# Performance work log

Measured on AMD Instinct MI355X. Metric: run time of the kernel, lower is better.

Reference implementation:

```python
import jax, jax.numpy as jnp
import numpy as np

DECAY = 0.9
EPS = 1e-5


def setup_inputs() -> dict:
    key = jax.random.key(0)
    k1, k2, k3 = jax.random.split(key, 3)
    N, D, K = 262144, 492, 40
    return {
        "inputs": jax.random.normal(k1, (N, D), dtype=jnp.float32),
        "embedding_weight": jax.random.normal(k2, (K, D), dtype=jnp.float32),
        "ema_w": jax.random.normal(k3, (K, D), dtype=jnp.float32),
        "ema_cluster_size": jnp.zeros((K,), dtype=jnp.float32),
    }


def reference(inputs, embedding_weight, ema_w, ema_cluster_size):
    K, D = embedding_weight.shape
    flat = inputs.reshape(-1, D)  # [N, D]
    # squared L2 distances to each codebook entry: [N, K]
    distances = (
        jnp.sum(flat * flat, axis=1, keepdims=True)
        + jnp.sum(embedding_weight * embedding_weight, axis=1)
        - 2.0 * flat @ embedding_weight.T
    )
    idx = jnp.argmin(distances, axis=1)  # [N] nearest-code indices
    # one-hot column sums == per-code counts; encodings.T @ flat == segment sum
    counts = jax.ops.segment_sum(jnp.ones_like(idx, dtype=flat.dtype), idx, num_segments=K)
    dw = jax.ops.segment_sum(flat, idx, num_segments=K)  # [K, D]
    # EMA cluster-size update + Laplace smoothing
    cs = ema_cluster_size * DECAY + (1.0 - DECAY) * counts
    n = jnp.sum(cs)
    cs = (cs + EPS) / (n + K * EPS) * n
    # EMA codebook weight update
    new_ema_w = ema_w * DECAY + (1.0 - DECAY) * dw
    new_embedding = new_ema_w / cs[:, None]
    # quantize with the UPDATED codebook (as the torch code does)
    quantized = new_embedding[idx].reshape(inputs.shape)
    loss_vq = jnp.mean((quantized - inputs) ** 2)
    return loss_vq
```

## Files before the change

### kernel.cpp

```cpp
#include <hip/hip_runtime.h>

#define D 492
#define KC 40
#define DECAY 0.9f
#define EPS 1e-5f
#define PSPREAD 64

typedef __attribute__((ext_vector_type(8))) short bf16x8;
typedef __attribute__((ext_vector_type(4))) float f32x4;

__device__ __forceinline__ unsigned short f2bf(float f) {
  unsigned u = __float_as_uint(f);
  return (unsigned short)((u + 0x7fffu + ((u >> 16) & 1u)) >> 16);
}

__global__ void vq_sqnorm(const float* __restrict__ emb, float* __restrict__ sq) {
  int k = blockIdx.x;
  int lane = threadIdx.x;
  float s = 0.f;
  for (int d = lane; d < D; d += 64) {
    float v = emb[k * D + d];
    s = fmaf(v, v, s);
  }
  #pragma unroll
  for (int off = 32; off; off >>= 1) s += __shfl_down(s, off, 64);
  if (lane == 0) sq[k] = s;
}

__global__ __launch_bounds__(256, 3) void vq_assign(
    const float* __restrict__ x, const float* __restrict__ emb,
    const float* __restrict__ sq, int* __restrict__ idxp,
    float* __restrict__ counts, float* __restrict__ sumsq) {
  __shared__ unsigned short As[256 * 40];
  __shared__ unsigned short Bs[48 * 40];
  __shared__ float sq_s[KC];
  __shared__ float lcnt[KC];
  __shared__ float lss[4];
  int t = threadIdx.x;
  long row0 = (long)blockIdx.x * 256;
  if (t < KC) { sq_s[t] = sq[t]; lcnt[t] = 0.f; }
  float ss = 0.f;
  f32x4 acc[4][3];
  #pragma unroll
  for (int m = 0; m < 4; m++)
    #pragma unroll
    for (int n = 0; n < 3; n++) acc[m][n] = (f32x4){0.f, 0.f, 0.f, 0.f};

  int w = t >> 6, L = t & 63;
  int lm = L & 15, kq = L >> 4;

  for (int step = 0; step < 16; step++) {
    int kbase = step * 32;
    #pragma unroll
    for (int i = 0; i < 8; i++) {
      int j = t + i * 256;
      int r = j >> 3, c4 = j & 7;
      int col = kbase + c4 * 4;
      float4 v = make_float4(0.f, 0.f, 0.f, 0.f);
      if (col < D) v = *(const float4*)&x[(row0 + r) * D + col];
      ss = fmaf(v.x, v.x, fmaf(v.y, v.y, fmaf(v.z, v.z, fmaf(v.w, v.w, ss))));
      ushort4 u = { f2bf(v.x), f2bf(v.y), f2bf(v.z), f2bf(v.w) };
      *(ushort4*)&As[r * 40 + c4 * 4] = u;
    }
    {
      int n = t >> 3, c4 = t & 7;
      int col = kbase + c4 * 4;
      float4 v = make_float4(0.f, 0.f, 0.f, 0.f);
      if (n < KC && col < D) v = *(const float4*)&emb[n * D + col];
      ushort4 u = { f2bf(v.x), f2bf(v.y), f2bf(v.z), f2bf(v.w) };
      *(ushort4*)&Bs[n * 40 + c4 * 4] = u;
      if (t < 128) {
        int j = t + 256;
        n = j >> 3; c4 = j & 7;
        col = kbase + c4 * 4;
        v = make_float4(0.f, 0.f, 0.f, 0.f);
        if (n < KC && col < D) v = *(const float4*)&emb[n * D + col];
        ushort4 u2 = { f2bf(v.x), f2bf(v.y), f2bf(v.z), f2bf(v.w) };
        *(ushort4*)&Bs[n * 40 + c4 * 4] = u2;
      }
    }
    __syncthreads();
    bf16x8 a[4], b[3];
    #pragma unroll
    for (int m = 0; m < 4; m++)
      a[m] = *(const bf16x8*)&As[(w * 64 + m * 16 + lm) * 40 + kq * 8];
    #pragma unroll
    for (int n = 0; n < 3; n++)
      b[n] = *(const bf16x8*)&Bs[(n * 16 + lm) * 40 + kq * 8];
    #pragma unroll
    for (int m = 0; m < 4; m++)
      #pragma unroll
      for (int n = 0; n < 3; n++)
        acc[m][n] = __builtin_amdgcn_mfma_f32_16x16x32_bf16(a[m], b[n], acc[m][n], 0, 0, 0);
    __syncthreads();
  }

  #pragma unroll
  for (int m = 0; m < 4; m++) {
    #pragma unroll
    for (int reg = 0; reg < 4; reg++) {
      float best = 3.4e38f; int bi = 0;
      #pragma unroll
      for (int n = 0; n < 3; n++) {
        int col = n * 16 + lm;
        if (col < KC) {
          float v = sq_s[col] - 2.f * acc[m][n][reg];
          if (v < best || (v == best && col < bi)) { best = v; bi = col; }
        }
      }
      #pragma unroll
      for (int off = 1; off < 16; off <<= 1) {
        float ov = __shfl_xor(best, off, 64);
        int oi = __shfl_xor(bi, off, 64);
        if (ov < best || (ov == best && oi < bi)) { best = ov; bi = oi; }
      }
      if (lm == 0) {
        int r = w * 64 + m * 16 + kq * 4 + reg;
        idxp[row0 + r] = bi;
        atomicAdd(&lcnt[bi], 1.f);
      }
    }
  }
  #pragma unroll
  for (int off = 32; off; off >>= 1) ss += __shfl_down(ss, off, 64);
  if (L == 0) lss[w] = ss;
  __syncthreads();
  if (t == 0) atomicAdd(sumsq, lss[0] + lss[1] + lss[2] + lss[3]);
  if (t < KC) atomicAdd(&counts[t], lcnt[t]);
}

__global__ __launch_bounds__(128) void vq_dw(
    const float* __restrict__ x, const int* __restrict__ idxp,
    float* __restrict__ dwp) {
  __shared__ int cnt[KC], base[KC], pos[KC];
  __shared__ unsigned short order[512];
  int t = threadIdx.x;
  long row0 = (long)blockIdx.x * 512;
  if (t < KC) cnt[t] = 0;
  __syncthreads();
  int myk[4];
  #pragma unroll
  for (int u = 0; u < 4; u++) {
    myk[u] = idxp[row0 + t + u * 128];
    atomicAdd(&cnt[myk[u]], 1);
  }
  __syncthreads();
  if (t == 0) {
    int s = 0;
    for (int k = 0; k < KC; k++) { base[k] = s; pos[k] = s; s += cnt[k]; }
  }
  __syncthreads();
  #pragma unroll
  for (int u = 0; u < 4; u++) {
    int p = atomicAdd(&pos[myk[u]], 1);
    order[p] = (unsigned short)((t + u * 128) | (myk[u] << 9));
  }
  __syncthreads();

  int c = 4 * t;
  bool act = c < D;
  float* dst = dwp + (long)(blockIdx.x & (PSPREAD - 1)) * (KC * D);
  float4 a = make_float4(0.f, 0.f, 0.f, 0.f);
  int kcur = -1;

  int pk[8], pk2[8];
  float4 v[8], v2[8];
  #pragma unroll
  for (int u = 0; u < 8; u++) pk[u] = order[u];
  #pragma unroll
  for (int u = 0; u < 8; u++)
    v[u] = act ? *(const float4*)&x[(row0 + (pk[u] & 511)) * D + c]
               : make_float4(0.f, 0.f, 0.f, 0.f);

  for (int j0 = 0; j0 < 512; j0 += 8) {
    if (j0 + 8 < 512) {
      #pragma unroll
      for (int u = 0; u < 8; u++) pk2[u] = order[j0 + 8 + u];
      #pragma unroll
      for (int u = 0; u < 8; u++)
        v2[u] = act ? *(const float4*)&x[(row0 + (pk2[u] & 511)) * D + c]
                    : make_float4(0.f, 0.f, 0.f, 0.f);
    }
    #pragma unroll
    for (int u = 0; u < 8; u++) {
      int k = pk[u] >> 9;
      if (k != kcur) {
        if (kcur >= 0 && act) {
          atomicAdd(&dst[kcur * D + c], a.x);
          atomicAdd(&dst[kcur * D + c + 1], a.y);
          atomicAdd(&dst[kcur * D + c + 2], a.z);
          atomicAdd(&dst[kcur * D + c + 3], a.w);
        }
        a = v[u]; kcur = k;
      } else {
        a.x += v[u].x; a.y += v[u].y; a.z += v[u].z; a.w += v[u].w;
      }
    }
    #pragma unroll
    for (int u = 0; u < 8; u++) { pk[u] = pk2[u]; v[u] = v2[u]; }
  }
  if (kcur >= 0 && act) {
    atomicAdd(&dst[kcur * D + c], a.x);
    atomicAdd(&dst[kcur * D + c + 1], a.y);
    atomicAdd(&dst[kcur * D + c + 2], a.z);
    atomicAdd(&dst[kcur * D + c + 3], a.w);
  }
}

__global__ __launch_bounds__(256) void vq_reduce(
    const float* __restrict__ dwp, float* __restrict__ dw) {
  int i = blockIdx.x * 256 + threadIdx.x;
  if (i >= KC * D) return;
  float s = 0.f;
  #pragma unroll 8
  for (int cpy = 0; cpy < PSPREAD; cpy++) s += dwp[cpy * (KC * D) + i];
  dw[i] = s;
}

__global__ __launch_bounds__(256) void vq_final(
    const float* __restrict__ ema_w, const float* __restrict__ ema_cs,
    const float* __restrict__ counts, const float* __restrict__ dw,
    const float* __restrict__ sumsq, float* __restrict__ out, long NDl) {
  __shared__ float lcs[KC], lcnt[KC];
  __shared__ float r1[4], r2[4];
  int t = threadIdx.x;
  if (t < KC) {
    float c = counts[t];
    lcnt[t] = c;
    lcs[t] = ema_cs[t] * DECAY + (1.f - DECAY) * c;
  }
  __syncthreads();
  if (t == 0) {
    float n = 0.f;
    for (int k = 0; k < KC; k++) n += lcs[k];
    for (int k = 0; k < KC; k++) lcs[k] = (lcs[k] + EPS) / (n + KC * EPS) * n;
  }
  __syncthreads();
  float t1 = 0.f, t2 = 0.f;
  for (int i = t; i < KC * D; i += 256) {
    float dwv = dw[i];
    int k = i / D;
    float E = (DECAY * ema_w[i] + (1.f - DECAY) * dwv) / lcs[k];
    t1 = fmaf(lcnt[k] * E, E, t1);
    t2 = fmaf(E, dwv, t2);
  }
  #pragma unroll
  for (int off = 32; off; off >>= 1) {
    t1 += __shfl_down(t1, off, 64);
    t2 += __shfl_down(t2, off, 64);
  }
  int lane = t & 63, w = t >> 6;
  if (lane == 0) { r1[w] = t1; r2[w] = t2; }
  __syncthreads();
  if (t == 0) {
    double T1 = (double)r1[0] + r1[1] + r1[2] + r1[3];
    double T2 = (double)r2[0] + r2[1] + r2[2] + r2[3];
    double L = ((double)sumsq[0] - 2.0 * T2 + T1) / (double)NDl;
    out[0] = (float)L;
  }
}

extern "C" void kernel_launch(void* const* d_in, const int* in_sizes, int n_in,
                              void* d_out, int out_size, void* d_ws, size_t ws_size,
                              hipStream_t stream) {
  const float* x = (const float*)d_in[0];
  const float* emb = (const float*)d_in[1];
  const float* ema_w = (const float*)d_in[2];
  const float* ema_cs = (const float*)d_in[3];
  float* out = (float*)d_out;
  long NDl = (long)in_sizes[0];
  int N = (int)(NDl / D);

  char* ws = (char*)d_ws;
  float* sq = (float*)ws;
  float* counts = (float*)(ws + 256);
  float* sumsq = (float*)(ws + 512);
  float* dw = (float*)(ws + 1024);
  size_t part_off = 1024 + (size_t)KC * D * 4;
  part_off = (part_off + 255) & ~(size_t)255;
  float* dwp = (float*)(ws + part_off);
  size_t idx_off = part_off + (size_t)PSPREAD * KC * D * 4;
  int* idxp = (int*)(ws + idx_off);

  hipMemsetAsync(ws + 256, 0, 768, stream);
  hipMemsetAsync(ws + part_off, 0, (size_t)PSPREAD * KC * D * 4, stream);

  vq_sqnorm<<<KC, 64, 0, stream>>>(emb, sq);
  vq_assign<<<N / 256, 256, 0, stream>>>(x, emb, sq, idxp, counts, sumsq);
  vq_dw<<<N / 512, 128, 0, stream>>>(x, idxp, dwp);
  vq_reduce<<<(KC * D + 255) / 256, 256, 0, stream>>>(dwp, dw);
  vq_final<<<1, 256, 0, stream>>>(ema_w, ema_cs, counts, dw, sumsq, out, NDl);
}
```

Baseline: 920.3 us.

## Load MFMA operands directly from global, pre-convert codebook to padded bf16

Adds a prep kernel that converts the codebook to a zero-padded bf16 layout (512 columns, 48 rows) alongside the squared norms. The assign kernel then drops its LDS staging and per-step barriers, with each lane loading its x fragment straight from global memory into registers and the B fragments from the pre-converted buffer. This removes shared-memory traffic, barriers and repeated fp32-to-bf16 conversion of the codebook. In exchange, x is read with strided, less coalesced per-lane accesses, and launch bounds are relaxed from 3 to 2 blocks per SM.

After: 1.128 ms. 1.23x slower.

```diff
diff --git a/kernel.cpp b/kernel.cpp
--- a/kernel.cpp
+++ b/kernel.cpp
@@ -14,31 +14,49 @@
   return (unsigned short)((u + 0x7fffu + ((u >> 16) & 1u)) >> 16);
 }
 
-__global__ void vq_sqnorm(const float* __restrict__ emb, float* __restrict__ sq) {
+__global__ void vq_prep(const float* __restrict__ emb, float* __restrict__ sq,
+                        unsigned short* __restrict__ embb) {
   int k = blockIdx.x;
   int lane = threadIdx.x;
+  int c0 = lane * 8;
   float s = 0.f;
-  for (int d = lane; d < D; d += 64) {
-    float v = emb[k * D + d];
-    s = fmaf(v, v, s);
-  }
+  float v[8];
+  #pragma unroll
+  for (int j = 0; j < 8; j++) {
+    int c = c0 + j;
+    float f = (k < KC && c < D) ? emb[k * D + c] : 0.f;
+    v[j] = f;
+    s = fmaf(f, f, s);
+  }
+  bf16x8 u;
+  #pragma unroll
+  for (int j = 0; j < 8; j++) u[j] = (short)f2bf(v[j]);
+  *(bf16x8*)&embb[k * 512 + c0] = u;
   #pragma unroll
   for (int off = 32; off; off >>= 1) s += __shfl_down(s, off, 64);
-  if (lane == 0) sq[k] = s;
-}
-
-__global__ __launch_bounds__(256, 3) void vq_assign(
-    const float* __restrict__ x, const float* __restrict__ emb,
+  if (k < KC && lane == 0) sq[k] = s;
+}
+
+__global__ __launch_bounds__(256, 2) void vq_assign(
+    const float* __restrict__ x, const unsigned short* __restrict__ embb,
     const float* __restrict__ sq, int* __restrict__ idxp,
     float* __restrict__ counts, float* __restrict__ sumsq) {
-  __shared__ unsigned short As[256 * 40];
-  __shared__ unsigned short Bs[48 * 40];
   __shared__ float sq_s[KC];
   __shared__ float lcnt[KC];
   __shared__ float lss[4];
   int t = threadIdx.x;
   long row0 = (long)blockIdx.x * 256;
   if (t < KC) { sq_s[t] = sq[t]; lcnt[t] = 0.f; }
+
+  int w = t >> 6, L = t & 63;
+  int lm = L & 15, kq = L >> 4;
+
+  const float* xr[4];
+  #pragma unroll
+  for (int m = 0; m < 4; m++)
+    xr[m] = x + (row0 + w * 64 + m * 16 + lm) * (long)D + kq * 8;
+  const unsigned short* bp = embb + lm * 512 + kq * 8;
+
   float ss = 0.f;
   f32x4 acc[4][3];
   #pragma unroll
@@ -46,54 +64,72 @@
     #pragma unroll
     for (int n = 0; n < 3; n++) acc[m][n] = (f32x4){0.f, 0.f, 0.f, 0.f};
 
-  int w = t >> 6, L = t & 63;
-  int lm = L & 15, kq = L >> 4;
-
-  for (int step = 0; step < 16; step++) {
-    int kbase = step * 32;
-    #pragma unroll
-    for (int i = 0; i < 8; i++) {
-      int j = t + i * 256;
-      int r = j >> 3, c4 = j & 7;
-      int col = kbase + c4 * 4;
-      float4 v = make_float4(0.f, 0.f, 0.f, 0.f);
-      if (col < D) v = *(const float4*)&x[(row0 + r) * D + col];
-      ss = fmaf(v.x, v.x, fmaf(v.y, v.y, fmaf(v.z, v.z, fmaf(v.w, v.w, ss))));
-      ushort4 u = { f2bf(v.x), f2bf(v.y), f2bf(v.z), f2bf(v.w) };
-      *(ushort4*)&As[r * 40 + c4 * 4] = u;
-    }
-    {
-      int n = t >> 3, c4 = t & 7;
-      int col = kbase + c4 * 4;
-      float4 v = make_float4(0.f, 0.f, 0.f, 0.f);
-      if (n < KC && col < D) v = *(const float4*)&emb[n * D + col];
-      ushort4 u = { f2bf(v.x), f2bf(v.y), f2bf(v.z), f2bf(v.w) };
-      *(ushort4*)&Bs[n * 40 + c4 * 4] = u;
-      if (t < 128) {
-        int j = t + 256;
-        n = j >> 3; c4 = j & 7;
-        col = kbase + c4 * 4;
-        v = make_float4(0.f, 0.f, 0.f, 0.f);
-        if (n < KC && col < D) v = *(const float4*)&emb[n * D + col];
-        ushort4 u2 = { f2bf(v.x), f2bf(v.y), f2bf(v.z), f2bf(v.w) };
-        *(ushort4*)&Bs[n * 40 + c4 * 4] = u2;
-      }
-    }
-    __syncthreads();
-    bf16x8 a[4], b[3];
-    #pragma unroll
-    for (int m = 0; m < 4; m++)
-      a[m] = *(const bf16x8*)&As[(w * 64 + m * 16 + lm) * 40 + kq * 8];
+  #pragma unroll 2
+  for (int step = 0; step < 15; step++) {
+    int c = step * 32;
+    float4 v0[4], v1[4];
+    #pragma unroll
+    for (int m = 0; m < 4; m++) {
+      v0[m] = *(const float4*)(xr[m] + c);
+      v1[m] = *(const float4*)(xr[m] + c + 4);
+    }
+    bf16x8 b[3];
     #pragma unroll
     for (int n = 0; n < 3; n++)
-      b[n] = *(const bf16x8*)&Bs[(n * 16 + lm) * 40 + kq * 8];
+      b[n] = *(const bf16x8*)(bp + n * 16 * 512 + c);
+    bf16x8 a[4];
+    #pragma unroll
+    for (int m = 0; m < 4; m++) {
+      ss = fmaf(v0[m].x, v0[m].x, fmaf(v0[m].y, v0[m].y,
+           fmaf(v0[m].z, v0[m].z, fmaf(v0[m].w, v0[m].w, ss))));
+      ss = fmaf(v1[m].x, v1[m].x, fmaf(v1[m].y, v1[m].y,
+           fmaf(v1[m].z, v1[m].z, fmaf(v1[m].w, v1[m].w, ss))));
+      a[m][0] = (short)f2bf(v0[m].x); a[m][1] = (short)f2bf(v0[m].y);
+      a[m][2] = (short)f2bf(v0[m].z); a[m][3] = (short)f2bf(v0[m].w);
+      a[m][4] = (short)f2bf(v1[m].x); a[m][5] = (short)f2bf(v1[m].y);
+      a[m][6] = (short)f2bf(v1[m].z); a[m][7] = (short)f2bf(v1[m].w);
+    }
     #pragma unroll
     for (int m = 0; m < 4; m++)
       #pragma unroll
       for (int n = 0; n < 3; n++)
         acc[m][n] = __builtin_amdgcn_mfma_f32_16x16x32_bf16(a[m], b[n], acc[m][n], 0, 0, 0);
-    __syncthreads();
-  }
+  }
+
+  {
+    int c = 480;
+    int cl = c + kq * 8;
+    float4 z = make_float4(0.f, 0.f, 0.f, 0.f);
+    float4 v0[4], v1[4];
+    #pragma unroll
+    for (int m = 0; m < 4; m++) {
+      v0[m] = (cl < D) ? *(const float4*)(xr[m] + c) : z;
+      v1[m] = (cl + 4 < D) ? *(const float4*)(xr[m] + c + 4) : z;
+    }
+    bf16x8 b[3];
+    #pragma unroll
+    for (int n = 0; n < 3; n++)
+      b[n] = *(const bf16x8*)(bp + n * 16 * 512 + c);
+    bf16x8 a[4];
+    #pragma unroll
+    for (int m = 0; m < 4; m++) {
+      ss = fmaf(v0[m].x, v0[m].x, fmaf(v0[m].y, v0[m].y,
+           fmaf(v0[m].z, v0[m].z, fmaf(v0[m].w, v0[m].w, ss))));
+      ss = fmaf(v1[m].x, v1[m].x, fmaf(v1[m].y, v1[m].y,
+           fmaf(v1[m].z, v1[m].z, fmaf(v1[m].w, v1[m].w, ss))));
+      a[m][0] = (short)f2bf(v0[m].x); a[m][1] = (short)f2bf(v0[m].y);
+      a[m][2] = (short)f2bf(v0[m].z); a[m][3] = (short)f2bf(v0[m].w);
+      a[m][4] = (short)f2bf(v1[m].x); a[m][5] = (short)f2bf(v1[m].y);
+      a[m][6] = (short)f2bf(v1[m].z); a[m][7] = (short)f2bf(v1[m].w);
+    }
+    #pragma unroll
+    for (int m = 0; m < 4; m++)
+      #pragma unroll
+      for (int n = 0; n < 3; n++)
+        acc[m][n] = __builtin_amdgcn_mfma_f32_16x16x32_bf16(a[m], b[n], acc[m][n], 0, 0, 0);
+  }
+
+  __syncthreads();
 
   #pragma unroll
   for (int m = 0; m < 4; m++) {
@@ -281,12 +317,14 @@
   float* dwp = (float*)(ws + part_off);
   size_t idx_off = part_off + (size_t)PSPREAD * KC * D * 4;
   int* idxp = (int*)(ws + idx_off);
+  size_t embb_off = idx_off + (size_t)N * 4;
+  unsigned short* embb = (unsigned short*)(ws + embb_off);
 
   hipMemsetAsync(ws + 256, 0, 768, stream);
   hipMemsetAsync(ws + part_off, 0, (size_t)PSPREAD * KC * D * 4, stream);
 
-  vq_sqnorm<<<KC, 64, 0, stream>>>(emb, sq);
-  vq_assign<<<N / 256, 256, 0, stream>>>(x, emb, sq, idxp, counts, sumsq);
+  vq_prep<<<48, 64, 0, stream>>>(emb, sq, embb);
+  vq_assign<<<N / 256, 256, 0, stream>>>(x, embb, sq, idxp, counts, sumsq);
   vq_dw<<<N / 512, 128, 0, stream>>>(x, idxp, dwp);
   vq_reduce<<<(KC * D + 255) / 256, 256, 0, stream>>>(dwp, dw);
   vq_final<<<1, 256, 0, stream>>>(ema_w, ema_cs, counts, dw, sumsq, out, NDl);
```
